# Optimization experiments

Measured on AMD Instinct MI355X. Metric: run time of the kernel, lower is better.

The kernel has to match this reference:

```python
import jax, jax.numpy as jnp
import numpy as np

DIM = 256; K = 3; PAD = 1; DIL = 1; B = 16; H = 56; W = 56
SP = 8           # share_planes
RADIX = 2
ATTN = max(DIM * RADIX // 4, 32)   # 128
EMB = K * K * DIM // SP            # 288

def conv(x, w, pad=0, dil=1, groups=1):
    return jax.lax.conv_general_dilated(
        x, w, (1, 1), [(pad, pad), (pad, pad)], rhs_dilation=(dil, dil),
        feature_group_count=groups, dimension_numbers=('NCHW', 'OIHW', 'NCHW'))

def bn(x, g, b, m, v, eps=1e-5):
    # eval-mode BatchNorm2d
    s = g * jax.lax.rsqrt(v + eps)
    return x * s[None, :, None, None] + (b - m * s)[None, :, None, None]

def gn(x, g, b, groups, eps=1e-5):
    Bb, C, Hh, Ww = x.shape
    xg = x.reshape(Bb, groups, C // groups, Hh, Ww)
    mu = xg.mean((2, 3, 4), keepdims=True)
    var = xg.var((2, 3, 4), keepdims=True)
    xg = (xg - mu) * jax.lax.rsqrt(var + eps)
    return xg.reshape(Bb, C, Hh, Ww) * g[None, :, None, None] + b[None, :, None, None]

def unfold3(x):
    # im2col for 3x3, stride 1, pad 1 -> (B, C, K*K, H, W)
    Bb, C, Hh, Ww = x.shape
    p = (K - 1) // 2
    xp = jnp.pad(x, ((0, 0), (0, 0), (p, p), (p, p)))
    return jnp.stack([xp[:, :, i:i + Hh, j:j + Ww] for i in range(K) for j in range(K)], axis=2)

def reference(x, ke_w, ke_g, ke_b, ke_m, ke_v, e1_w, e1_g, e1_b, e1_m, e1_v,
              e2_w, e2_b, gng, gnb, c1_w, c1_g, c1_b, c1_m, c1_v,
              b2_g, b2_b, b2_m, b2_v, s1_w, s1_b, s1_g, s1_bb, s1_m, s1_v,
              s2_w, s2_b):
    Bb = x.shape[0]
    # key embed: grouped kxk conv + BN + ReLU
    k = jax.nn.relu(bn(conv(x, ke_w, pad=PAD, dil=DIL, groups=4), ke_g, ke_b, ke_m, ke_v))
    qk = jnp.concatenate([x, k], axis=1)                     # (B, 2*DIM, H, W)
    # dynamic kernel branch
    wemb = jax.nn.relu(bn(conv(qk, e1_w), e1_g, e1_b, e1_m, e1_v))
    wemb = conv(wemb, e2_w) + e2_b[None, :, None, None]
    wemb = gn(wemb, gng, gnb, DIM // SP)                     # GroupNorm(dim//8 groups)
    wemb = wemb.reshape(Bb, DIM // SP, K * K, H, W)
    # value branch
    xq = bn(conv(x, c1_w), c1_g, c1_b, c1_m, c1_v)
    # local dynamic convolution: per-pixel kernel shared across SP channels
    patches = unfold3(xq).reshape(Bb, DIM // SP, SP, K * K, H, W)
    y = (patches * wemb[:, :, None]).sum(3).reshape(Bb, DIM, H, W)
    y = bn(y, b2_g, b2_b, b2_m, b2_v)
    y = y * jax.nn.sigmoid(y)                                # swish
    # split attention over radix=2 branches (y, k)
    xs = jnp.stack([y, k], axis=2)                           # (B, C, 2, H, W)
    gap = xs.sum(2).mean((2, 3), keepdims=True)              # (B, C, 1, 1)
    a = jax.nn.relu(bn(conv(gap, s1_w) + s1_b[None, :, None, None], s1_g, s1_bb, s1_m, s1_v))
    a = conv(a, s2_w) + s2_b[None, :, None, None]            # (B, 2*C, 1, 1)
    a = jax.nn.softmax(a.reshape(Bb, DIM, RADIX), axis=2)
    out = (xs * a[:, :, :, None, None]).sum(2)
    return out

def setup_inputs():
    key = jax.random.key(0)
    ks = iter(jax.random.split(key, 40))
    def n(shape, s=1.0):
        return jax.random.normal(next(ks), shape, jnp.float32) * s
    def u(shape):
        return jax.random.uniform(next(ks), shape, jnp.float32, minval=0.5, maxval=1.5)
    d = {}
    d['x'] = n((B, DIM, H, W))
    d['ke_w'] = n((DIM, DIM // 4, K, K), 0.05)
    d['ke_g'] = u((DIM,)); d['ke_b'] = n((DIM,), 0.1); d['ke_m'] = n((DIM,), 0.1); d['ke_v'] = u((DIM,))
    d['e1_w'] = n((DIM // 2, 2 * DIM, 1, 1), 0.05)
    d['e1_g'] = u((DIM // 2,)); d['e1_b'] = n((DIM // 2,), 0.1); d['e1_m'] = n((DIM // 2,), 0.1); d['e1_v'] = u((DIM // 2,))
    d['e2_w'] = n((EMB, DIM // 2, 1, 1), 0.05); d['e2_b'] = n((EMB,), 0.1)
    d['gng'] = u((EMB,)); d['gnb'] = n((EMB,), 0.1)
    d['c1_w'] = n((DIM, DIM, 1, 1), 0.05)
    d['c1_g'] = u((DIM,)); d['c1_b'] = n((DIM,), 0.1); d['c1_m'] = n((DIM,), 0.1); d['c1_v'] = u((DIM,))
    d['b2_g'] = u((DIM,)); d['b2_b'] = n((DIM,), 0.1); d['b2_m'] = n((DIM,), 0.1); d['b2_v'] = u((DIM,))
    d['s1_w'] = n((ATTN, DIM, 1, 1), 0.05); d['s1_b'] = n((ATTN,), 0.1)
    d['s1_g'] = u((ATTN,)); d['s1_bb'] = n((ATTN,), 0.1); d['s1_m'] = n((ATTN,), 0.1); d['s1_v'] = u((ATTN,))
    d['s2_w'] = n((RADIX * DIM, ATTN, 1, 1), 0.05); d['s2_b'] = n((RADIX * DIM,), 0.1)
    return d
```

## Files before the change

kernel.cpp:

```cpp
#include <hip/hip_runtime.h>
#include <hip/hip_bf16.h>

typedef __hip_bfloat16 bf16;
typedef float f32x4 __attribute__((ext_vector_type(4)));
typedef short s16x8 __attribute__((ext_vector_type(8)));

#define NPIX 3136
#define HDIM 56
#define CDIM 256
#define PPIX 3364

static __device__ __forceinline__ float b2f(bf16 v){ return __bfloat162float(v); }
static __device__ __forceinline__ bf16  f2b(float v){ return __float2bfloat16(v); }

#define O_KE_S 0
#define O_KE_B 256
#define O_E1_S 512
#define O_E1_B 640
#define O_C1_S 768
#define O_C1_B 1024
#define O_B2_S 1280
#define O_B2_B 1536
#define O_S1_S 1792
#define O_S1_B 1920
#define O_E2B  2048
#define O_GNS  2336
#define O_GAP  3360
#define O_ATT  7456
#define O_SA   15872

__global__ __launch_bounds__(256) void preconv(
    const float* __restrict__ x,
    const float* __restrict__ kew, const float* __restrict__ e1w,
    const float* __restrict__ e2w, const float* __restrict__ c1w,
    const float* keg, const float* keb, const float* kem, const float* kev,
    const float* e1g, const float* e1b, const float* e1m, const float* e1v,
    const float* e2b,
    const float* c1g, const float* c1b, const float* c1m, const float* c1v,
    const float* b2g, const float* b2b, const float* b2m, const float* b2v,
    const float* s1g, const float* s1bb, const float* s1m, const float* s1v,
    bf16* kewT, bf16* e1wb, bf16* e2wb, bf16* c1wb, float* o,
    bf16* xh, bf16* xq)
{
    int bid = blockIdx.x, t = threadIdx.x;
    __shared__ bf16 T[64][72];
    if (bid >= 2165) {
        int cbid = bid - 2165;
        int px = cbid % 49;
        int r = cbid / 49;
        int cy = r & 3, b = r >> 2;
        int c0 = cy * 64, p0 = px * 64;
        #pragma unroll
        for (int it = 0; it < 4; it++) {
            int slot = t + it * 256;
            int cl = slot >> 4, ch4 = slot & 15;
            float4 v = *(const float4*)(x + ((long)b * CDIM + c0 + cl) * NPIX + p0 + ch4 * 4);
            T[ch4 * 4 + 0][cl] = f2b(v.x);
            T[ch4 * 4 + 1][cl] = f2b(v.y);
            T[ch4 * 4 + 2][cl] = f2b(v.z);
            T[ch4 * 4 + 3][cl] = f2b(v.w);
        }
        __syncthreads();
        #pragma unroll
        for (int it = 0; it < 2; it++) {
            int slot = t + it * 256;
            int p = slot >> 3, cc = slot & 7;
            int pl = p0 + p;
            int h = pl / HDIM, w = pl - h * HDIM;
            *(float4*)(xh + ((long)b * PPIX + (h + 1) * 58 + (w + 1)) * 256 + c0 + cc * 8) = *(const float4*)&T[p][cc * 8];
        }
        return;
    }
    if (bid < 576) {
        int i = bid * 256 + t;
        int ci = i & 63, co_l = (i >> 6) & 63;
        int gt = i >> 12;
        int tap = gt % 9, g = gt / 9;
        int co = g * 64 + co_l;
        kewT[i] = f2b(kew[(co * 64 + ci) * 9 + tap]);
    } else if (bid < 832) {
        int i = (bid - 576) * 256 + t; e1wb[i] = f2b(e1w[i]);
    } else if (bid < 976) {
        int i = (bid - 832) * 256 + t; e2wb[i] = f2b(e2w[i]);
    } else if (bid < 1232) {
        int i = (bid - 976) * 256 + t; c1wb[i] = f2b(c1w[i]);
    } else if (bid == 1232) {
        const float eps = 1e-5f;
        {
            float s = keg[t] * rsqrtf(kev[t] + eps);
            o[O_KE_S + t] = s; o[O_KE_B + t] = keb[t] - kem[t] * s;
            s = c1g[t] * rsqrtf(c1v[t] + eps);
            o[O_C1_S + t] = s; o[O_C1_B + t] = c1b[t] - c1m[t] * s;
            s = b2g[t] * rsqrtf(b2v[t] + eps);
            o[O_B2_S + t] = s; o[O_B2_B + t] = b2b[t] - b2m[t] * s;
        }
        if (t < 128) {
            float s = e1g[t] * rsqrtf(e1v[t] + eps);
            o[O_E1_S + t] = s; o[O_E1_B + t] = e1b[t] - e1m[t] * s;
            s = s1g[t] * rsqrtf(s1v[t] + eps);
            o[O_S1_S + t] = s; o[O_S1_B + t] = s1bb[t] - s1m[t] * s;
        }
        for (int i = t; i < 288; i += 256) o[O_E2B + i] = e2b[i];
    } else if (bid < 1253) {
        int j = (bid - 1233) * 256 + t;
        if (j < 1024) o[O_GNS + j] = 0.f;
        else if (j < 5120) o[O_GAP + j - 1024] = 0.f;
    } else {
        int j = (bid - 1253) * 256 + t;
        bf16* arr = (j >= 116736) ? xq : xh;
        int r = j % 116736;
        int img = r / 7296;
        int s = r % 7296;
        int pi = s >> 5, cc = s & 31;
        int pos;
        if (pi < 58)       pos = pi;
        else if (pi < 116) pos = 57 * 58 + (pi - 58);
        else if (pi < 172) pos = (pi - 115) * 58;
        else               pos = (pi - 171) * 58 + 57;
        float4 z = {0.f, 0.f, 0.f, 0.f};
        *(float4*)(arr + ((long)img * PPIX + pos) * 256 + cc * 8) = z;
    }
}

__global__ __launch_bounds__(256) void gconv_c1(
    const bf16* __restrict__ xp, const bf16* __restrict__ wT,
    const float* __restrict__ kes, const float* __restrict__ keb,
    const bf16* __restrict__ c1w,
    const float* __restrict__ c1s, const float* __restrict__ c1b,
    bf16* __restrict__ kh, bf16* __restrict__ xq, float* __restrict__ gap)
{
    __shared__ bf16 SH[232 * 64];
    int b = blockIdx.z;
    int bx = blockIdx.x;
    int t = threadIdx.x;
    int wv = t >> 6, lane = t & 63, q = lane >> 4, ln = lane & 15;

    if (bx < 112) {
        int hx = bx >> 2, g = bx & 3;
        int h0 = hx * 2;
        bf16* As = SH;
        #pragma unroll
        for (int i = 0; i < 8; i++) {
            int slot = t + i * 256;
            if (slot < 1856) {
                int pos = slot >> 3, chunkL = slot & 7;
                int ri = pos / 58, ci = pos - ri * 58;
                int chunkg = chunkL ^ (pos & 7);
                float4 v = *(const float4*)(xp + (((long)b * PPIX + (h0 + ri) * 58 + ci) * 256 + g * 64 + chunkg * 8));
                *(float4*)&SH[pos * 64 + chunkL * 8] = v;
            }
        }
        int posb[7];
        #pragma unroll
        for (int pt = 0; pt < 7; pt++) {
            int p = pt * 16 + ln;
            int prow = (p >= 56) ? 1 : 0;
            int pcol = p - prow * 56;
            posb[pt] = prow * 58 + pcol + 1;
        }
        const bf16* wbase = wT + ((long)(g * 9) * 64 + wv * 16 + ln) * 64;
        __syncthreads();

        f32x4 acc[7] = {};
        #pragma unroll
        for (int tap = 0; tap < 9; tap++) {
            const int dr = tap / 3;
            const int dc = tap % 3 - 1;
            const bf16* wq = wbase + tap * 64 * 64;
            s16x8 B0 = *(const s16x8*)(wq + q * 8);
            s16x8 B1 = *(const s16x8*)(wq + 32 + q * 8);
            #pragma unroll
            for (int pt = 0; pt < 7; pt++) {
                int pos = posb[pt] + dr * 58 + dc;
                int off0 = pos * 64 + ((q ^ (pos & 7)) * 8);
                s16x8 a0 = *(const s16x8*)&As[off0];
                s16x8 a1 = *(const s16x8*)&As[off0 ^ 32];
                acc[pt] = __builtin_amdgcn_mfma_f32_16x16x32_bf16(a0, B0, acc[pt], 0, 0, 0);
                acc[pt] = __builtin_amdgcn_mfma_f32_16x16x32_bf16(a1, B1, acc[pt], 0, 0, 0);
            }
        }
        __syncthreads();
        bf16* T = As;
        int co = g * 64 + wv * 16 + ln;
        float sc = kes[co], bi = keb[co];
        #pragma unroll
        for (int pt = 0; pt < 7; pt++)
            #pragma unroll
            for (int r = 0; r < 4; r++)
                T[(pt * 16 + q * 4 + r) * 72 + wv * 16 + ln] = f2b(fmaxf(acc[pt][r] * sc + bi, 0.f));
        __syncthreads();
        int pimg0 = hx * 112;
        #pragma unroll
        for (int i = 0; i < 4; i++) {
            int slot = t + i * 256;
            if (slot < 896) {
                int row = slot >> 3, cc = slot & 7;
                *(float4*)(kh + ((long)b * NPIX + pimg0 + row) * CDIM + g * 64 + cc * 8) = *(const float4*)&T[row * 72 + cc * 8];
            }
        }
        {
            int co_l = t & 63, rb = t >> 6;
            float s = 0.f;
            #pragma unroll
            for (int r = 0; r < 28; r++) s += b2f(T[(rb * 28 + r) * 72 + co_l]);
            atomicAdd(&gap[b * 256 + g * 64 + co_l], s);
        }
    } else {
        int px = bx - 112;
        int mt = px & 1; px >>= 1;
        int p0 = px * 64;
        int m0 = mt * 128;
        bf16* As = SH;
        bf16* Bs = SH + 64 * 72;

        f32x4 acc[4][2] = {};
        for (int k0 = 0; k0 < 256; k0 += 64) {
            __syncthreads();
            #pragma unroll
            for (int i = 0; i < 2; i++) {
                int slot = t + i * 256;
                int chunk = slot & 7, row = slot >> 3;
                long pp = p0 + row;
                long pidx = (long)b * PPIX + pp + 2 * (pp / HDIM) + 59;
                *(float4*)&As[row * 72 + chunk * 8] = *(const float4*)(xp + pidx * 256 + k0 + chunk * 8);
            }
            #pragma unroll
            for (int i = 0; i < 4; i++) {
                int slot = t + i * 256;
                int chunk = slot & 7, row = slot >> 3;
                *(float4*)&Bs[row * 72 + chunk * 8] = *(const float4*)(c1w + (long)(m0 + row) * 256 + k0 + chunk * 8);
            }
            __syncthreads();
            #pragma unroll
            for (int kk = 0; kk < 2; kk++) {
                s16x8 a[4];
                #pragma unroll
                for (int pt = 0; pt < 4; pt++)
                    a[pt] = *(const s16x8*)&As[(pt * 16 + ln) * 72 + kk * 32 + q * 8];
                #pragma unroll
                for (int mi = 0; mi < 2; mi++) {
                    s16x8 bb = *(const s16x8*)&Bs[(wv * 32 + mi * 16 + ln) * 72 + kk * 32 + q * 8];
                    #pragma unroll
                    for (int pt = 0; pt < 4; pt++)
                        acc[pt][mi] = __builtin_amdgcn_mfma_f32_16x16x32_bf16(a[pt], bb, acc[pt][mi], 0, 0, 0);
                }
            }
        }
        __syncthreads();
        bf16* T = SH;
        #pragma unroll
        for (int mi = 0; mi < 2; mi++) {
            int m = m0 + wv * 32 + mi * 16 + ln;
            float sc = c1s[m], bi = c1b[m];
            #pragma unroll
            for (int pt = 0; pt < 4; pt++) {
                #pragma unroll
                for (int r = 0; r < 4; r++) {
                    float v = acc[pt][mi][r] * sc + bi;
                    T[(pt * 16 + q * 4 + r) * 144 + wv * 32 + mi * 16 + ln] = f2b(v);
                }
            }
        }
        __syncthreads();
        #pragma unroll
        for (int i = 0; i < 4; i++) {
            int slot = t + i * 256;
            int row = slot >> 4, chunk = slot & 15;
            long pp = p0 + row;
            long pidx = (long)b * PPIX + pp + 2 * (pp / HDIM) + 59;
            *(float4*)(xq + pidx * 256 + m0 + chunk * 8) = *(const float4*)&T[row * 144 + chunk * 8];
        }
    }
}

__global__ __launch_bounds__(256) void mfma_gemm_e1(
    const bf16* __restrict__ Wt, const bf16* __restrict__ X0, const bf16* __restrict__ X1,
    const float* __restrict__ scale, const float* __restrict__ bias,
    bf16* __restrict__ Y)
{
    int b = blockIdx.y;
    int p0 = blockIdx.x * 64;
    __shared__ bf16 SH[64 * 72 + 128 * 72];
    bf16* As = SH;
    bf16* Bs = SH + 64 * 72;
    int t = threadIdx.x;
    int wv = t >> 6, lane = t & 63, q = lane >> 4, ln = lane & 15;

    f32x4 acc[4][2] = {};
    for (int k0 = 0; k0 < 512; k0 += 64) {
        __syncthreads();
        #pragma unroll
        for (int i = 0; i < 2; i++) {
            int slot = t + i * 256;
            int chunk = slot & 7, row = slot >> 3;
            int ch = k0 + chunk * 8;
            const bf16* src;
            if (ch < 256) {
                long pp = p0 + row;
                long pidx = (long)b * PPIX + pp + 2 * (pp / HDIM) + 59;
                src = X0 + pidx * 256 + ch;
            } else {
                src = X1 + ((long)b * NPIX + p0 + row) * 256 + (ch - 256);
            }
            *(float4*)&As[row * 72 + chunk * 8] = *(const float4*)src;
        }
        #pragma unroll
        for (int i = 0; i < 4; i++) {
            int slot = t + i * 256;
            int chunk = slot & 7, row = slot >> 3;
            *(float4*)&Bs[row * 72 + chunk * 8] = *(const float4*)(Wt + (long)row * 512 + k0 + chunk * 8);
        }
        __syncthreads();
        #pragma unroll
        for (int kk = 0; kk < 2; kk++) {
            s16x8 a[4];
            #pragma unroll
            for (int pt = 0; pt < 4; pt++)
                a[pt] = *(const s16x8*)&As[(pt * 16 + ln) * 72 + kk * 32 + q * 8];
            #pragma unroll
            for (int mi = 0; mi < 2; mi++) {
                s16x8 bb = *(const s16x8*)&Bs[(wv * 32 + mi * 16 + ln) * 72 + kk * 32 + q * 8];
                #pragma unroll
                for (int pt = 0; pt < 4; pt++)
                    acc[pt][mi] = __builtin_amdgcn_mfma_f32_16x16x32_bf16(a[pt], bb, acc[pt][mi], 0, 0, 0);
            }
        }
    }
    __syncthreads();
    bf16* T = SH;
    #pragma unroll
    for (int mi = 0; mi < 2; mi++) {
        int m = wv * 32 + mi * 16 + ln;
        float sc = scale[m], bi = bias[m];
        #pragma unroll
        for (int pt = 0; pt < 4; pt++) {
            #pragma unroll
            for (int r = 0; r < 4; r++) {
                float v = fmaxf(acc[pt][mi][r] * sc + bi, 0.f);
                T[(pt * 16 + q * 4 + r) * 144 + m] = f2b(v);
            }
        }
    }
    __syncthreads();
    #pragma unroll
    for (int i = 0; i < 4; i++) {
        int slot = t + i * 256;
        int row = slot >> 4, chunk = slot & 15;
        *(float4*)(Y + ((long)b * NPIX + p0 + row) * 128 + chunk * 8) = *(const float4*)&T[row * 144 + chunk * 8];
    }
}

__global__ __launch_bounds__(256) void mfma_gemm_e2(
    const bf16* __restrict__ Wt, const bf16* __restrict__ X0,
    const float* __restrict__ bias,
    bf16* __restrict__ Y, float* __restrict__ gnsum)
{
    const int K = 128, M = 288;
    int b = blockIdx.z;
    int p0 = blockIdx.x * 64;
    int m0 = blockIdx.y * 128;
    __shared__ bf16 SH[64 * 72 + 128 * 72];
    bf16* As = SH;
    bf16* Bs = SH + 64 * 72;
    __shared__ float gs[64];
    int t = threadIdx.x;
    int wv = t >> 6, lane = t & 63, q = lane >> 4, ln = lane & 15;
    if (t < 64) gs[t] = 0.f;

    f32x4 acc[4][2] = {};
    for (int k0 = 0; k0 < K; k0 += 64) {
        __syncthreads();
        #pragma unroll
        for (int i = 0; i < 2; i++) {
            int slot = t + i * 256;
            int chunk = slot & 7, row = slot >> 3;
            int ch = k0 + chunk * 8;
            *(float4*)&As[row * 72 + chunk * 8] = *(const float4*)(X0 + ((long)b * NPIX + p0 + row) * K + ch);
        }
        #pragma unroll
        for (int i = 0; i < 4; i++) {
            int slot = t + i * 256;
            int chunk = slot & 7, row = slot >> 3;
            int m = m0 + row;
            float4 v = {0.f, 0.f, 0.f, 0.f};
            if (m < M) v = *(const float4*)(Wt + (long)m * K + k0 + chunk * 8);
            *(float4*)&Bs[row * 72 + chunk * 8] = v;
        }
        __syncthreads();
        #pragma unroll
        for (int kk = 0; kk < 2; kk++) {
            s16x8 a[4];
            #pragma unroll
            for (int pt = 0; pt < 4; pt++)
                a[pt] = *(const s16x8*)&As[(pt * 16 + ln) * 72 + kk * 32 + q * 8];
            #pragma unroll
            for (int mi = 0; mi < 2; mi++) {
                s16x8 bb = *(const s16x8*)&Bs[(wv * 32 + mi * 16 + ln) * 72 + kk * 32 + q * 8];
                #pragma unroll
                for (int pt = 0; pt < 4; pt++)
                    acc[pt][mi] = __builtin_amdgcn_mfma_f32_16x16x32_bf16(a[pt], bb, acc[pt][mi], 0, 0, 0);
            }
        }
    }

    __syncthreads();
    bf16* T = SH;
    #pragma unroll
    for (int mi = 0; mi < 2; mi++) {
        int m = m0 + wv * 32 + mi * 16 + ln;
        int mc = (m > M - 1) ? (M - 1) : m;
        float bi = bias[mc];
        float ps = 0.f, pq = 0.f;
        #pragma unroll
        for (int pt = 0; pt < 4; pt++) {
            #pragma unroll
            for (int r = 0; r < 4; r++) {
                float v = acc[pt][mi][r] + bi;
                ps += v; pq += v * v;
                T[(pt * 16 + q * 4 + r) * 144 + wv * 32 + mi * 16 + ln] = f2b(v);
            }
        }
        if (m < M) {
            int grp = m / 9;
            atomicAdd(&gs[grp * 2], ps);
            atomicAdd(&gs[grp * 2 + 1], pq);
        }
    }
    __syncthreads();
    #pragma unroll
    for (int i = 0; i < 4; i++) {
        int slot = t + i * 256;
        int chunk = slot & 15, row = slot >> 4;
        int m = m0 + chunk * 8;
        if (m + 8 <= M)
            *(float4*)(Y + ((long)b * NPIX + p0 + row) * M + m) = *(const float4*)&T[row * 144 + chunk * 8];
    }
    if (t < 64) atomicAdd(&gnsum[b * 64 + t], gs[t]);
}

__global__ void gnfold(const float* __restrict__ gnsum,
                       const float* __restrict__ gng, const float* __restrict__ gnb,
                       float* __restrict__ o)
{
    int b = blockIdx.x, t = threadIdx.x;
    for (int s = t; s < 288; s += 256) {
        int g2 = s / 9;
        float S = gnsum[b * 64 + g2 * 2], Q = gnsum[b * 64 + g2 * 2 + 1];
        float mu = S * (1.f / 28224.f);
        float var = Q * (1.f / 28224.f) - mu * mu;
        float rs = rsqrtf(fmaxf(var, 0.f) + 1e-5f);
        float a = rs * gng[s];
        o[O_SA + b * 576 + s] = a;
        o[O_SA + b * 576 + 288 + s] = gnb[s] - mu * a;
    }
}

__global__ __launch_bounds__(256) void dynconv(
    const bf16* __restrict__ xq, const bf16* __restrict__ wemb,
    const float* __restrict__ fold,
    const float* __restrict__ b2s, const float* __restrict__ b2b,
    bf16* __restrict__ y, float* __restrict__ gap)
{
    int t = threadIdx.x;
    int grp = t & 31, pl = t >> 5;
    int bid = blockIdx.x;
    int b = bid / 392;
    int p0 = (bid - b * 392) * 8;
    int p = p0 + pl;
    int h = p / HDIM, w = p - h * HDIM;

    __shared__ bf16 WE[2304];
    __shared__ float SAB[576];
    __shared__ float R[8][256];

    {
        const bf16* src = wemb + (long)(b * NPIX + p0) * 288;
        #pragma unroll
        for (int i = 0; i < 2; i++) {
            int s = t + i * 256;
            if (s < 288) *(float4*)&WE[s * 8] = *(const float4*)(src + s * 8);
        }
    }
    {
        const float4* src = (const float4*)(fold + O_SA + b * 576);
        if (t < 144) ((float4*)SAB)[t] = src[t];
    }
    __syncthreads();

    long base = ((long)b * PPIX + (h + 1) * 58 + (w + 1)) * 256 + grp * 8;
    const bf16* rm = xq + base - 58 * 256;
    const bf16* rc = xq + base;
    const bf16* rq = xq + base + 58 * 256;
    s16x8 xv[9];
    xv[0] = *(const s16x8*)(rm - 256); xv[1] = *(const s16x8*)rm; xv[2] = *(const s16x8*)(rm + 256);
    xv[3] = *(const s16x8*)(rc - 256); xv[4] = *(const s16x8*)rc; xv[5] = *(const s16x8*)(rc + 256);
    xv[6] = *(const s16x8*)(rq - 256); xv[7] = *(const s16x8*)rq; xv[8] = *(const s16x8*)(rq + 256);

    float acc[8] = {};
    #pragma unroll
    for (int tp = 0; tp < 9; tp++) {
        int wi = grp * 9 + tp;
        float wt = b2f(WE[pl * 288 + wi]) * SAB[wi] + SAB[288 + wi];
        const bf16* xb = (const bf16*)&xv[tp];
        #pragma unroll
        for (int i = 0; i < 8; i++) acc[i] += b2f(xb[i]) * wt;
    }

    bf16 outv[8];
    float sv[8];
    #pragma unroll
    for (int i = 0; i < 8; i++) {
        int c = grp * 8 + i;
        float v = acc[i] * b2s[c] + b2b[c];
        float sw = v / (1.f + __expf(-v));
        sv[i] = sw;
        outv[i] = f2b(sw);
    }
    *(float4*)(y + ((long)b * NPIX + p) * CDIM + grp * 8) = *(const float4*)outv;

    #pragma unroll
    for (int i = 0; i < 8; i++) R[pl][grp * 8 + i] = sv[i];
    __syncthreads();
    float s = 0.f;
    #pragma unroll
    for (int j = 0; j < 8; j++) s += R[j][t];
    atomicAdd(&gap[b * 256 + t], s);
}

__global__ void attnk(const float* __restrict__ gap,
                      const float* __restrict__ s1w, const float* __restrict__ s1b,
                      const float* __restrict__ s1s, const float* __restrict__ s1bi,
                      const float* __restrict__ s2w, const float* __restrict__ s2b,
                      float* __restrict__ att)
{
    int b = blockIdx.x, t = threadIdx.x;
    __shared__ float g[256], a1[128];
    for (int i = t; i < 256; i += 128) g[i] = gap[b * 256 + i] * (1.f / NPIX);
    __syncthreads();
    float s = 0.f;
    for (int ci = 0; ci < 256; ci++) s += s1w[t * 256 + ci] * g[ci];
    s += s1b[t];
    s = s * s1s[t] + s1bi[t];
    a1[t] = fmaxf(s, 0.f);
    __syncthreads();
    for (int c = t; c < 256; c += 128) {
        float v0 = s2b[2 * c], v1 = s2b[2 * c + 1];
        for (int ci = 0; ci < 128; ci++) {
            float av = a1[ci];
            v0 += s2w[(2 * c) * 128 + ci] * av;
            v1 += s2w[(2 * c + 1) * 128 + ci] * av;
        }
        float m = fmaxf(v0, v1);
        float e0 = __expf(v0 - m), e1 = __expf(v1 - m);
        float inv = 1.f / (e0 + e1);
        att[(b * 256 + c) * 2 + 0] = e0 * inv;
        att[(b * 256 + c) * 2 + 1] = e1 * inv;
    }
}

__global__ __launch_bounds__(256) void finalk(
    const bf16* __restrict__ y, const bf16* __restrict__ k,
    const float* __restrict__ att, float* __restrict__ out)
{
    int b = blockIdx.z, c0 = blockIdx.y * 64, p0 = blockIdx.x * 64;
    __shared__ bf16 Ys[64][72], Ks[64][72];
    int t = threadIdx.x;
    #pragma unroll
    for (int i = 0; i < 2; i++) {
        int slot = t + i * 256;
        int row = slot >> 3, cc = slot & 7;
        long off = ((long)b * NPIX + p0 + row) * CDIM + c0 + cc * 8;
        *(float4*)&Ys[row][cc * 8] = *(const float4*)(y + off);
        *(float4*)&Ks[row][cc * 8] = *(const float4*)(k + off);
    }
    __syncthreads();
    int c_l = t >> 2, pc = t & 3;
    int c = c0 + c_l;
    float a0 = att[(b * 256 + c) * 2], a1 = att[(b * 256 + c) * 2 + 1];
    float4 o[4];
    float* of = (float*)o;
    #pragma unroll
    for (int j = 0; j < 16; j++) {
        int p = pc * 16 + j;
        of[j] = b2f(Ys[p][c_l]) * a0 + b2f(Ks[p][c_l]) * a1;
    }
    float* dst = out + ((long)b * CDIM + c) * NPIX + p0 + pc * 16;
    #pragma unroll
    for (int j = 0; j < 4; j++) ((float4*)dst)[j] = o[j];
}

extern "C" void kernel_launch(void* const* d_in, const int* in_sizes, int n_in,
                              void* d_out, int out_size, void* d_ws, size_t ws_size,
                              hipStream_t stream)
{
    const float* x    = (const float*)d_in[0];
    const float* ke_w = (const float*)d_in[1];
    const float* ke_g = (const float*)d_in[2];
    const float* ke_b = (const float*)d_in[3];
    const float* ke_m = (const float*)d_in[4];
    const float* ke_v = (const float*)d_in[5];
    const float* e1_w = (const float*)d_in[6];
    const float* e1_g = (const float*)d_in[7];
    const float* e1_b = (const float*)d_in[8];
    const float* e1_m = (const float*)d_in[9];
    const float* e1_v = (const float*)d_in[10];
    const float* e2_w = (const float*)d_in[11];
    const float* e2_b = (const float*)d_in[12];
    const float* gng  = (const float*)d_in[13];
    const float* gnb  = (const float*)d_in[14];
    const float* c1_w = (const float*)d_in[15];
    const float* c1_g = (const float*)d_in[16];
    const float* c1_b = (const float*)d_in[17];
    const float* c1_m = (const float*)d_in[18];
    const float* c1_v = (const float*)d_in[19];
    const float* b2_g = (const float*)d_in[20];
    const float* b2_b = (const float*)d_in[21];
    const float* b2_m = (const float*)d_in[22];
    const float* b2_v = (const float*)d_in[23];
    const float* s1_w = (const float*)d_in[24];
    const float* s1_b = (const float*)d_in[25];
    const float* s1_g = (const float*)d_in[26];
    const float* s1_bb= (const float*)d_in[27];
    const float* s1_m = (const float*)d_in[28];
    const float* s1_v = (const float*)d_in[29];
    const float* s2_w = (const float*)d_in[30];
    const float* s2_b = (const float*)d_in[31];

    float* fold = (float*)d_ws;
    bf16* wsb   = (bf16*)((char*)d_ws + 131072);
    bf16* xh   = wsb;
    bf16* kh   = xh + 13778944L;
    bf16* wemb = kh + 12845056L;
    bf16* w1   = wemb + 14450688L;
    bf16* kewT = w1 + 6422528L;
    bf16* e1wb = kewT + 147456L;
    bf16* e2wb = e1wb + 65536L;
    bf16* c1wb = e2wb + 36864L;
    bf16* xq   = c1wb + 65536L;
    bf16* yb   = xh;

    preconv<<<dim3(5301), dim3(256), 0, stream>>>(
        x, ke_w, e1_w, e2_w, c1_w,
        ke_g, ke_b, ke_m, ke_v, e1_g, e1_b, e1_m, e1_v, e2_b,
        c1_g, c1_b, c1_m, c1_v, b2_g, b2_b, b2_m, b2_v,
        s1_g, s1_bb, s1_m, s1_v,
        kewT, e1wb, e2wb, c1wb, fold, xh, xq);

    gconv_c1<<<dim3(210, 1, 16), dim3(256), 0, stream>>>(
        xh, kewT, fold + O_KE_S, fold + O_KE_B,
        c1wb, fold + O_C1_S, fold + O_C1_B,
        kh, xq, fold + O_GAP);

    mfma_gemm_e1<<<dim3(49, 16), dim3(256), 0, stream>>>(
        e1wb, xh, kh, fold + O_E1_S, fold + O_E1_B, w1);

    mfma_gemm_e2<<<dim3(49, 3, 16), dim3(256), 0, stream>>>(
        e2wb, w1, fold + O_E2B, wemb, fold + O_GNS);

    gnfold<<<dim3(16), dim3(256), 0, stream>>>(fold + O_GNS, gng, gnb, fold);

    dynconv<<<dim3(6272), dim3(256), 0, stream>>>(
        xq, wemb, fold, fold + O_B2_S, fold + O_B2_B, yb, fold + O_GAP);

    attnk<<<dim3(16), dim3(128), 0, stream>>>(
        fold + O_GAP, s1_w, s1_b, fold + O_S1_S, fold + O_S1_B, s2_w, s2_b, fold + O_ATT);

    finalk<<<dim3(49, 4, 16), dim3(256), 0, stream>>>(yb, kh, fold + O_ATT, (float*)d_out);
}
```

Before: 326.2 us.

## Fuse e1 and e2 pointwise GEMMs, keeping intermediate activations in LDS

Merges the two chained 1x1-conv GEMM kernels into one. Each block computes its 64-pixel tile of the 128-channel ReLU'd e1 output, keeps it in shared memory, then loops over three 128-wide output tiles of e2 with GroupNorm partial sums. This removes the global round-trip of the w1 intermediate and one launch. In exchange, grid parallelism drops from 49x3x16 to 49x16 blocks for the e2 stage, and LDS use per block grows.

```diff
diff --git a/kernel.cpp b/kernel.cpp
--- a/kernel.cpp
+++ b/kernel.cpp
@@ -273,167 +273,148 @@
     }
 }
 
-__global__ __launch_bounds__(256) void mfma_gemm_e1(
-    const bf16* __restrict__ Wt, const bf16* __restrict__ X0, const bf16* __restrict__ X1,
-    const float* __restrict__ scale, const float* __restrict__ bias,
-    bf16* __restrict__ Y)
+__global__ __launch_bounds__(256) void mfma_e12(
+    const bf16* __restrict__ e1w, const bf16* __restrict__ e2w,
+    const bf16* __restrict__ X0, const bf16* __restrict__ X1,
+    const float* __restrict__ e1s, const float* __restrict__ e1b,
+    const float* __restrict__ e2bias,
+    bf16* __restrict__ Y, float* __restrict__ gnsum)
 {
     int b = blockIdx.y;
     int p0 = blockIdx.x * 64;
-    __shared__ bf16 SH[64 * 72 + 128 * 72];
-    bf16* As = SH;
-    bf16* Bs = SH + 64 * 72;
-    int t = threadIdx.x;
-    int wv = t >> 6, lane = t & 63, q = lane >> 4, ln = lane & 15;
-
-    f32x4 acc[4][2] = {};
-    for (int k0 = 0; k0 < 512; k0 += 64) {
-        __syncthreads();
-        #pragma unroll
-        for (int i = 0; i < 2; i++) {
-            int slot = t + i * 256;
-            int chunk = slot & 7, row = slot >> 3;
-            int ch = k0 + chunk * 8;
-            const bf16* src;
-            if (ch < 256) {
-                long pp = p0 + row;
-                long pidx = (long)b * PPIX + pp + 2 * (pp / HDIM) + 59;
-                src = X0 + pidx * 256 + ch;
-            } else {
-                src = X1 + ((long)b * NPIX + p0 + row) * 256 + (ch - 256);
-            }
-            *(float4*)&As[row * 72 + chunk * 8] = *(const float4*)src;
-        }
-        #pragma unroll
-        for (int i = 0; i < 4; i++) {
-            int slot = t + i * 256;
-            int chunk = slot & 7, row = slot >> 3;
-            *(float4*)&Bs[row * 72 + chunk * 8] = *(const float4*)(Wt + (long)row * 512 + k0 + chunk * 8);
-        }
-        __syncthreads();
-        #pragma unroll
-        for (int kk = 0; kk < 2; kk++) {
-            s16x8 a[4];
-            #pragma unroll
-            for (int pt = 0; pt < 4; pt++)
-                a[pt] = *(const s16x8*)&As[(pt * 16 + ln) * 72 + kk * 32 + q * 8];
-            #pragma unroll
-            for (int mi = 0; mi < 2; mi++) {
-                s16x8 bb = *(const s16x8*)&Bs[(wv * 32 + mi * 16 + ln) * 72 + kk * 32 + q * 8];
-                #pragma unroll
-                for (int pt = 0; pt < 4; pt++)
-                    acc[pt][mi] = __builtin_amdgcn_mfma_f32_16x16x32_bf16(a[pt], bb, acc[pt][mi], 0, 0, 0);
-            }
-        }
-    }
-    __syncthreads();
-    bf16* T = SH;
-    #pragma unroll
-    for (int mi = 0; mi < 2; mi++) {
-        int m = wv * 32 + mi * 16 + ln;
-        float sc = scale[m], bi = bias[m];
-        #pragma unroll
-        for (int pt = 0; pt < 4; pt++) {
-            #pragma unroll
-            for (int r = 0; r < 4; r++) {
-                float v = fmaxf(acc[pt][mi][r] * sc + bi, 0.f);
-                T[(pt * 16 + q * 4 + r) * 144 + m] = f2b(v);
-            }
-        }
-    }
-    __syncthreads();
-    #pragma unroll
-    for (int i = 0; i < 4; i++) {
-        int slot = t + i * 256;
-        int row = slot >> 4, chunk = slot & 15;
-        *(float4*)(Y + ((long)b * NPIX + p0 + row) * 128 + chunk * 8) = *(const float4*)&T[row * 144 + chunk * 8];
-    }
-}
-
-__global__ __launch_bounds__(256) void mfma_gemm_e2(
-    const bf16* __restrict__ Wt, const bf16* __restrict__ X0,
-    const float* __restrict__ bias,
-    bf16* __restrict__ Y, float* __restrict__ gnsum)
-{
-    const int K = 128, M = 288;
-    int b = blockIdx.z;
-    int p0 = blockIdx.x * 64;
-    int m0 = blockIdx.y * 128;
-    __shared__ bf16 SH[64 * 72 + 128 * 72];
-    bf16* As = SH;
-    bf16* Bs = SH + 64 * 72;
+    __shared__ bf16 SH[17920];
     __shared__ float gs[64];
     int t = threadIdx.x;
     int wv = t >> 6, lane = t & 63, q = lane >> 4, ln = lane & 15;
     if (t < 64) gs[t] = 0.f;
 
-    f32x4 acc[4][2] = {};
-    for (int k0 = 0; k0 < K; k0 += 64) {
-        __syncthreads();
-        #pragma unroll
-        for (int i = 0; i < 2; i++) {
-            int slot = t + i * 256;
-            int chunk = slot & 7, row = slot >> 3;
-            int ch = k0 + chunk * 8;
-            *(float4*)&As[row * 72 + chunk * 8] = *(const float4*)(X0 + ((long)b * NPIX + p0 + row) * K + ch);
-        }
-        #pragma unroll
-        for (int i = 0; i < 4; i++) {
-            int slot = t + i * 256;
-            int chunk = slot & 7, row = slot >> 3;
-            int m = m0 + row;
-            float4 v = {0.f, 0.f, 0.f, 0.f};
-            if (m < M) v = *(const float4*)(Wt + (long)m * K + k0 + chunk * 8);
-            *(float4*)&Bs[row * 72 + chunk * 8] = v;
-        }
-        __syncthreads();
-        #pragma unroll
-        for (int kk = 0; kk < 2; kk++) {
-            s16x8 a[4];
-            #pragma unroll
-            for (int pt = 0; pt < 4; pt++)
-                a[pt] = *(const s16x8*)&As[(pt * 16 + ln) * 72 + kk * 32 + q * 8];
+    {
+        bf16* As = SH;
+        bf16* Bs = SH + 4608;
+        f32x4 acc[4][2] = {};
+        for (int k0 = 0; k0 < 512; k0 += 64) {
+            __syncthreads();
+            #pragma unroll
+            for (int i = 0; i < 2; i++) {
+                int slot = t + i * 256;
+                int chunk = slot & 7, row = slot >> 3;
+                int ch = k0 + chunk * 8;
+                const bf16* src;
+                if (ch < 256) {
+                    long pp = p0 + row;
+                    long pidx = (long)b * PPIX + pp + 2 * (pp / HDIM) + 59;
+                    src = X0 + pidx * 256 + ch;
+                } else {
+                    src = X1 + ((long)b * NPIX + p0 + row) * 256 + (ch - 256);
+                }
+                *(float4*)&As[row * 72 + chunk * 8] = *(const float4*)src;
+            }
+            #pragma unroll
+            for (int i = 0; i < 4; i++) {
+                int slot = t + i * 256;
+                int chunk = slot & 7, row = slot >> 3;
+                *(float4*)&Bs[row * 72 + chunk * 8] = *(const float4*)(e1w + (long)row * 512 + k0 + chunk * 8);
+            }
+            __syncthreads();
+            #pragma unroll
+            for (int kk = 0; kk < 2; kk++) {
+                s16x8 a[4];
+                #pragma unroll
+                for (int pt = 0; pt < 4; pt++)
+                    a[pt] = *(const s16x8*)&As[(pt * 16 + ln) * 72 + kk * 32 + q * 8];
+                #pragma unroll
+                for (int mi = 0; mi < 2; mi++) {
+                    s16x8 bb = *(const s16x8*)&Bs[(wv * 32 + mi * 16 + ln) * 72 + kk * 32 + q * 8];
+                    #pragma unroll
+                    for (int pt = 0; pt < 4; pt++)
+                        acc[pt][mi] = __builtin_amdgcn_mfma_f32_16x16x32_bf16(a[pt], bb, acc[pt][mi], 0, 0, 0);
+                }
+            }
+        }
+        __syncthreads();
+        bf16* W1 = SH;
+        #pragma unroll
+        for (int mi = 0; mi < 2; mi++) {
+            int m = wv * 32 + mi * 16 + ln;
+            float sc = e1s[m], bi = e1b[m];
+            #pragma unroll
+            for (int pt = 0; pt < 4; pt++) {
+                #pragma unroll
+                for (int r = 0; r < 4; r++) {
+                    float v = fmaxf(acc[pt][mi][r] * sc + bi, 0.f);
+                    W1[(pt * 16 + q * 4 + r) * 136 + m] = f2b(v);
+                }
+            }
+        }
+        __syncthreads();
+    }
+
+    {
+        bf16* W1 = SH;
+        bf16* Bs = SH + 8704;
+        for (int mt = 0; mt < 3; mt++) {
+            int m0 = mt * 128;
+            f32x4 acc[4][2] = {};
+            for (int k0 = 0; k0 < 128; k0 += 64) {
+                __syncthreads();
+                #pragma unroll
+                for (int i = 0; i < 4; i++) {
+                    int slot = t + i * 256;
+                    int chunk = slot & 7, row = slot >> 3;
+                    int m = m0 + row;
+                    float4 v = {0.f, 0.f, 0.f, 0.f};
+                    if (m < 288) v = *(const float4*)(e2w + (long)m * 128 + k0 + chunk * 8);
+                    *(float4*)&Bs[row * 72 + chunk * 8] = v;
+                }
+                __syncthreads();
+                #pragma unroll
+                for (int kk = 0; kk < 2; kk++) {
+                    s16x8 a[4];
+                    #pragma unroll
+                    for (int pt = 0; pt < 4; pt++)
+                        a[pt] = *(const s16x8*)&W1[(pt * 16 + ln) * 136 + k0 + kk * 32 + q * 8];
+                    #pragma unroll
+                    for (int mi = 0; mi < 2; mi++) {
+                        s16x8 bb = *(const s16x8*)&Bs[(wv * 32 + mi * 16 + ln) * 72 + kk * 32 + q * 8];
+                        #pragma unroll
+                        for (int pt = 0; pt < 4; pt++)
+                            acc[pt][mi] = __builtin_amdgcn_mfma_f32_16x16x32_bf16(a[pt], bb, acc[pt][mi], 0, 0, 0);
+                    }
+                }
+            }
+            __syncthreads();
+            bf16* T = Bs;
             #pragma unroll
             for (int mi = 0; mi < 2; mi++) {
-                s16x8 bb = *(const s16x8*)&Bs[(wv * 32 + mi * 16 + ln) * 72 + kk * 32 + q * 8];
-                #pragma unroll
-                for (int pt = 0; pt < 4; pt++)
-                    acc[pt][mi] = __builtin_amdgcn_mfma_f32_16x16x32_bf16(a[pt], bb, acc[pt][mi], 0, 0, 0);
-            }
-        }
-    }
-
-    __syncthreads();
-    bf16* T = SH;
-    #pragma unroll
-    for (int mi = 0; mi < 2; mi++) {
-        int m = m0 + wv * 32 + mi * 16 + ln;
-        int mc = (m > M - 1) ? (M - 1) : m;
-        float bi = bias[mc];
-        float ps = 0.f, pq = 0.f;
-        #pragma unroll
-        for (int pt = 0; pt < 4; pt++) {
-            #pragma unroll
-            for (int r = 0; r < 4; r++) {
-                float v = acc[pt][mi][r] + bi;
-                ps += v; pq += v * v;
-                T[(pt * 16 + q * 4 + r) * 144 + wv * 32 + mi * 16 + ln] = f2b(v);
-            }
-        }
-        if (m < M) {
-            int grp = m / 9;
-            atomicAdd(&gs[grp * 2], ps);
-            atomicAdd(&gs[grp * 2 + 1], pq);
-        }
-    }
-    __syncthreads();
-    #pragma unroll
-    for (int i = 0; i < 4; i++) {
-        int slot = t + i * 256;
-        int chunk = slot & 15, row = slot >> 4;
-        int m = m0 + chunk * 8;
-        if (m + 8 <= M)
-            *(float4*)(Y + ((long)b * NPIX + p0 + row) * M + m) = *(const float4*)&T[row * 144 + chunk * 8];
+                int m = m0 + wv * 32 + mi * 16 + ln;
+                int mc = (m > 287) ? 287 : m;
+                float bi = e2bias[mc];
+                float ps = 0.f, pq = 0.f;
+                #pragma unroll
+                for (int pt = 0; pt < 4; pt++) {
+                    #pragma unroll
+                    for (int r = 0; r < 4; r++) {
+                        float v = acc[pt][mi][r] + bi;
+                        ps += v; pq += v * v;
+                        T[(pt * 16 + q * 4 + r) * 144 + wv * 32 + mi * 16 + ln] = f2b(v);
+                    }
+                }
+                if (m < 288) {
+                    int grp = m / 9;
+                    atomicAdd(&gs[grp * 2], ps);
+                    atomicAdd(&gs[grp * 2 + 1], pq);
+                }
+            }
+            __syncthreads();
+            #pragma unroll
+            for (int i = 0; i < 4; i++) {
+                int slot = t + i * 256;
+                int chunk = slot & 15, row = slot >> 4;
+                int m = m0 + chunk * 8;
+                if (m + 8 <= 288)
+                    *(float4*)(Y + ((long)b * NPIX + p0 + row) * 288 + m) = *(const float4*)&T[row * 144 + chunk * 8];
+            }
+        }
     }
     if (t < 64) atomicAdd(&gnsum[b * 64 + t], gs[t]);
 }
@@ -631,8 +612,7 @@
     bf16* xh   = wsb;
     bf16* kh   = xh + 13778944L;
     bf16* wemb = kh + 12845056L;
-    bf16* w1   = wemb + 14450688L;
-    bf16* kewT = w1 + 6422528L;
+    bf16* kewT = wemb + 14450688L;
     bf16* e1wb = kewT + 147456L;
     bf16* e2wb = e1wb + 65536L;
     bf16* c1wb = e2wb + 36864L;
@@ -651,11 +631,9 @@
         c1wb, fold + O_C1_S, fold + O_C1_B,
         kh, xq, fold + O_GAP);
 
-    mfma_gemm_e1<<<dim3(49, 16), dim3(256), 0, stream>>>(
-        e1wb, xh, kh, fold + O_E1_S, fold + O_E1_B, w1);
-
-    mfma_gemm_e2<<<dim3(49, 3, 16), dim3(256), 0, stream>>>(
-        e2wb, w1, fold + O_E2B, wemb, fold + O_GNS);
+    mfma_e12<<<dim3(49, 16), dim3(256), 0, stream>>>(
+        e1wb, e2wb, xh, kh, fold + O_E1_S, fold + O_E1_B, fold + O_E2B,
+        wemb, fold + O_GNS);
 
     gnfold<<<dim3(16), dim3(256), 0, stream>>>(fold + O_GNS, gng, gnb, fold);
 
```

Result: no change. 325.0 us (-0.4%).
